# Kernel optimization log

Hardware: AMD Instinct MI355X
Metric: run time of the kernel (lower is better)

Reference implementation:

```python
import jax, jax.numpy as jnp
import numpy as np
from math import factorial

# irreps as (mul, l, parity): hidden = 64x0e + 32x1o + 16x2e (dim 240), edge = 1x0e + 1x1o (dim 4)
HIDDEN = [(64, 0, 1), (32, 1, -1), (16, 2, 1)]
EDGE = [(1, 0, 1), (1, 1, -1)]
N_LAYERS = 6
N_NODES = 10000
N_EDGES = 160000
N_GRAPHS = 64
IN_DIM = 3
LATENT = 128  # config.LATENT_DIM_GNN
W_STD = 0.1   # weight scale keeps 6 residual bilinear layers numerically stable

def _dim(ir):
    return sum(m * (2 * l + 1) for m, l, _ in ir)

def _slices(ir):
    out, o = [], 0
    for m, l, _ in ir:
        d = m * (2 * l + 1)
        out.append(slice(o, o + d))
        o += d
    return out

def _cg(j1, m1, j2, m2, j3, m3):
    # Condon-Shortley Clebsch-Gordan <j1 m1 j2 m2 | j3 m3> (Racah formula)
    if m1 + m2 != m3:
        return 0.0
    f = lambda n: float(factorial(n))
    pre = ((2 * j3 + 1) * f(j3 + j1 - j2) * f(j3 - j1 + j2) * f(j1 + j2 - j3) / f(j1 + j2 + j3 + 1)) ** 0.5
    pre *= (f(j3 + m3) * f(j3 - m3) * f(j1 - m1) * f(j1 + m1) * f(j2 - m2) * f(j2 + m2)) ** 0.5
    s = 0.0
    for k in range(j1 + j2 - j3 + 1):
        a = [k, j1 + j2 - j3 - k, j1 - m1 - k, j2 + m2 - k, j3 - j2 + m1 + k, j3 - j1 - m2 + k]
        if any(t < 0 for t in a):
            continue
        s += (-1) ** k / np.prod([f(t) for t in a])
    return pre * s

def _w3j_complex(l1, l2, l3):
    W = np.zeros((2 * l1 + 1, 2 * l2 + 1, 2 * l3 + 1))
    for m1 in range(-l1, l1 + 1):
        for m2 in range(-l2, l2 + 1):
            m3 = -(m1 + m2)
            if abs(m3) > l3:
                continue
            W[m1 + l1, m2 + l2, m3 + l3] = (-1) ** (l1 - l2 - m3) / np.sqrt(2 * l3 + 1) * _cg(l1, m1, l2, m2, l3, -m3)
    return W

def _A_real(l):
    # real SH in terms of complex SH: Y^r_m = sum_mu A[m, mu] Y_mu
    A = np.zeros((2 * l + 1, 2 * l + 1), dtype=complex)
    A[l, l] = 1.0
    for m in range(1, l + 1):
        A[l + m, l + m] = (-1) ** m / np.sqrt(2)
        A[l + m, l - m] = 1 / np.sqrt(2)
        A[l - m, l + m] = -1j * (-1) ** m / np.sqrt(2)
        A[l - m, l - m] = 1j / np.sqrt(2)
    return A

_W3J_CACHE = {}
def real_w3j(l1, l2, l3):
    key = (l1, l2, l3)
    if key not in _W3J_CACHE:
        T = np.einsum('ad,be,cf,def->abc', _A_real(l1), _A_real(l2), _A_real(l3), _w3j_complex(l1, l2, l3).astype(complex))
        T = np.real(T)  # exactly real when l1+l2+l3 is even (true for all paths here)
        _W3J_CACHE[key] = (T / np.linalg.norm(T)).astype(np.float32)
    return _W3J_CACHE[key]

def _paths(ir1, ir2, irout):
    ps = []
    for i1, (_, l1, p1) in enumerate(ir1):
        for i2, (_, l2, p2) in enumerate(ir2):
            for i3, (_, l3, p3) in enumerate(irout):
                if p3 == p1 * p2 and abs(l1 - l2) <= l3 <= l1 + l2:
                    ps.append((i1, i2, i3))
    return ps

MSG_PATHS = _paths(HIDDEN, EDGE, HIDDEN)
UPD_PATHS = _paths(HIDDEN, HIDDEN, HIDDEN)

def _tp_wsize(ir1, ir2, irout, paths):
    return sum(ir1[a][0] * ir2[b][0] * irout[c][0] for a, b, c in paths)

MSG_WSIZE = _tp_wsize(HIDDEN, EDGE, HIDDEN, MSG_PATHS)
UPD_WSIZE = _tp_wsize(HIDDEN, HIDDEN, HIDDEN, UPD_PATHS)
LIN_WSIZE = sum(m * m for m, _, _ in HIDDEN)

def tensor_product(x1, x2, w_flat, ir1, ir2, irout, paths):
    # FullyConnectedTensorProduct: per-path CG-coupled bilinear op with path normalization
    s1, s2, s3 = _slices(ir1), _slices(ir2), _slices(irout)
    npo = [0] * len(irout)
    for _, _, i3 in paths:
        npo[i3] += 1
    out = jnp.zeros((x1.shape[0], _dim(irout)), dtype=x1.dtype)
    off = 0
    for i1, i2, i3 in paths:
        m1, l1, _ = ir1[i1]; m2, l2, _ = ir2[i2]; m3, l3, _ = irout[i3]
        W = w_flat[off:off + m1 * m2 * m3].reshape(m1, m2, m3)
        off += m1 * m2 * m3
        C = jnp.asarray(real_w3j(l1, l2, l3), dtype=x1.dtype)
        a = x1[:, s1[i1]].reshape(-1, m1, 2 * l1 + 1)
        b = x2[:, s2[i2]].reshape(-1, m2, 2 * l2 + 1)
        alpha = 1.0 / np.sqrt(m1 * m2 * npo[i3])
        y = alpha * jnp.einsum('nui,nvj,uvw,ijk->nwk', a, b, W, C)
        out = out.at[:, s3[i3]].add(y.reshape(-1, m3 * (2 * l3 + 1)))
    return out

def irreps_linear(x, w_flat, ir):
    # e3nn Linear with identical in/out irreps: per-irrep mixing of multiplicities
    sl = _slices(ir)
    parts, off = [], 0
    for i, (m, l, _) in enumerate(ir):
        W = w_flat[off:off + m * m].reshape(m, m)
        off += m * m
        xi = x[:, sl[i]].reshape(-1, m, 2 * l + 1)
        parts.append((jnp.einsum('nui,uv->nvi', xi, W) / np.sqrt(m)).reshape(-1, m * (2 * l + 1)))
    return jnp.concatenate(parts, axis=-1)

def _forward(x, pos, w_init, w_tp_msg, w_lin_msg, w_tp_upd, w_lin_upd, w_final, edge_index, batch):
    row, col = edge_index[0], edge_index[1]
    r_vec = pos[row] - pos[col]                           # (E, 3)
    dist = jnp.linalg.norm(r_vec, axis=-1, keepdims=True)
    nvec = r_vec / jnp.maximum(dist, 1e-8)
    edge_attr = jnp.concatenate([dist, nvec], axis=-1)    # layer consumes [dist, r_vec] = 1x0e + 1x1o
    h = jnp.zeros((x.shape[0], _dim(HIDDEN)), dtype=x.dtype)
    h = h.at[:, :64].set(x @ w_init / np.sqrt(IN_DIM))    # initial Linear hits only 0e channels
    for L in range(N_LAYERS):
        hj = h[col]  # gather neighbor (source) features
        msg = tensor_product(hj, edge_attr, w_tp_msg[L], HIDDEN, EDGE, HIDDEN, MSG_PATHS) \
            + irreps_linear(hj, w_lin_msg[L], HIDDEN)
        agg = jax.ops.segment_sum(msg, row, num_segments=N_NODES)  # scatter-add aggregate
        upd = tensor_product(h, agg, w_tp_upd[L], HIDDEN, HIDDEN, HIDDEN, UPD_PATHS) \
            + irreps_linear(h, w_lin_upd[L], HIDDEN)
        h = h + upd  # residual
    scal = h[:, :64]  # 0e (invariant) channels
    cnt = jax.ops.segment_sum(jnp.ones((x.shape[0],), x.dtype), batch, num_segments=N_GRAPHS)
    pooled = jax.ops.segment_sum(scal, batch, num_segments=N_GRAPHS) / jnp.maximum(cnt, 1.0)[:, None]
    return pooled @ w_final / np.sqrt(64)

def setup_inputs() -> dict:
    key = jax.random.key(0)
    ks = jax.random.split(key, 10)
    return {
        'x': jax.random.normal(ks[0], (N_NODES, IN_DIM), jnp.float32),
        'pos': jax.random.normal(ks[1], (N_NODES, 3), jnp.float32),
        'w_init': jax.random.normal(ks[2], (IN_DIM, 64), jnp.float32),
        'w_tp_msg': jax.random.normal(ks[3], (N_LAYERS, MSG_WSIZE), jnp.float32) * W_STD,
        'w_lin_msg': jax.random.normal(ks[4], (N_LAYERS, LIN_WSIZE), jnp.float32) * W_STD,
        'w_tp_upd': jax.random.normal(ks[5], (N_LAYERS, UPD_WSIZE), jnp.float32) * W_STD,
        'w_lin_upd': jax.random.normal(ks[6], (N_LAYERS, LIN_WSIZE), jnp.float32) * W_STD,
        'w_final': jax.random.normal(ks[7], (64, LATENT), jnp.float32),
        'edge_index': jax.random.randint(ks[8], (2, N_EDGES), 0, N_NODES),
        'batch': jnp.sort(jax.random.randint(ks[9], (N_NODES,), 0, N_GRAPHS)),
    }

def reference(x, pos, w_init, w_tp_msg, w_lin_msg, w_tp_upd, w_lin_upd, w_final, edge_index, batch):
    return _forward(x, pos, w_init, w_tp_msg, w_lin_msg, w_tp_upd, w_lin_upd, w_final, edge_index, batch)
```

## Files before the change

### kernel.cpp

```cpp
#include <hip/hip_runtime.h>
#include <cmath>
#include <cstring>
#include <complex>

#define NN 10000
#define NE 160000
#define HD 240
#define ZD 912
#define NG 64
#define MSG_WS 10496
#define UPD_WS 561152
#define LIN_WS 5376

struct CMsgPre { float a000, a011, a110, a112, a211; float c101[9]; float c202[25]; };
struct CEdge   { float c011[9]; float c110[9]; float c112[45]; float c211[45]; };
struct CUpdS   { float s000; float c011[9]; float c022[25]; float c101[9]; float c202[25]; };
struct CUpdD   { float c110[9]; float c220[25]; };
struct CUpdP   { float c112[45]; float c121[45]; float c211[45]; float c222[125]; };


__global__ __launch_bounds__(256) void k_edge_attr(
    const float* __restrict__ pos, const int* __restrict__ ei, CEdge C,
    float* __restrict__ EA, float* __restrict__ CN) {
  int e = blockIdx.x * 256 + threadIdx.x;
  if (e >= NE) return;
  int r = ei[e], c = ei[NE + e];
  float dx = pos[r*3+0] - pos[c*3+0];
  float dy = pos[r*3+1] - pos[c*3+1];
  float dz = pos[r*3+2] - pos[c*3+2];
  float d = sqrtf(dx*dx + dy*dy + dz*dz);
  float inv = 1.0f / fmaxf(d, 1e-8f);
  float n0 = dx*inv, n1 = dy*inv, n2 = dz*inv;
  EA[e*4+0] = d; EA[e*4+1] = n0; EA[e*4+2] = n1; EA[e*4+3] = n2;
  float* cn = CN + (size_t)e*36;
#pragma unroll
  for (int k = 0; k < 3; k++)
    cn[k] = n0*C.c011[0*3+k] + n1*C.c011[1*3+k] + n2*C.c011[2*3+k];
#pragma unroll
  for (int i = 0; i < 3; i++)
    cn[3+i] = n0*C.c110[i*3+0] + n1*C.c110[i*3+1] + n2*C.c110[i*3+2];
#pragma unroll
  for (int i = 0; i < 3; i++)
#pragma unroll
    for (int k = 0; k < 5; k++)
      cn[6+i*5+k] = n0*C.c112[(i*3+0)*5+k] + n1*C.c112[(i*3+1)*5+k] + n2*C.c112[(i*3+2)*5+k];
#pragma unroll
  for (int i = 0; i < 5; i++)
#pragma unroll
    for (int k = 0; k < 3; k++)
      cn[21+i*3+k] = n0*C.c211[(i*3+0)*3+k] + n1*C.c211[(i*3+1)*3+k] + n2*C.c211[(i*3+2)*3+k];
}

__global__ __launch_bounds__(256) void k_h_init(
    const float* __restrict__ x, const float* __restrict__ wi, float* __restrict__ HT) {
  int n = blockIdx.x * 256 + threadIdx.x;
  int e = blockIdx.y;
  if (n >= NN) return;
  float v = 0.f;
  if (e < 64)
    v = (x[n*3+0]*wi[0*64+e] + x[n*3+1]*wi[64+e] + x[n*3+2]*wi[128+e]) * 0.57735026918962576f;
  HT[e*NN + n] = v;
}

__global__ __launch_bounds__(256) void k_node_pre(
    const float* __restrict__ HT, const float* __restrict__ Wm, const float* __restrict__ Wl,
    CMsgPre C, float* __restrict__ Z) {
  int n = blockIdx.x * 256 + threadIdx.x;
  int widx = blockIdx.y;
  if (n >= NN) return;
  float acc = 0.f;
  if (widx < 64) {
    int w = widx;
    for (int u = 0; u < 64; u++) acc += HT[u*NN+n] * Wm[u*64+w];
    acc *= C.a000;
  } else if (widx < 96) {
    int w = widx - 64;
    for (int u = 0; u < 64; u++) acc += HT[u*NN+n] * Wm[4096 + u*32+w];
    acc *= C.a011;
  } else if (widx < 192) {
    int t = widx - 96, w = t/3, k = t - w*3;
    for (int u = 0; u < 32; u++) {
      float g = HT[(64+u*3+0)*NN+n]*C.c101[0*3+k]
              + HT[(64+u*3+1)*NN+n]*C.c101[1*3+k]
              + HT[(64+u*3+2)*NN+n]*C.c101[2*3+k];
      acc += Wm[6144 + u*32+w] * g;
    }
  } else if (widx < 384) {
    int t = widx - 192, w = t/3, i = t - w*3;
    for (int u = 0; u < 32; u++) acc += HT[(64+u*3+i)*NN+n] * Wm[7168 + u*64+w];
    acc *= C.a110;
  } else if (widx < 432) {
    int t = widx - 384, w = t/3, i = t - w*3;
    for (int u = 0; u < 32; u++) acc += HT[(64+u*3+i)*NN+n] * Wm[9216 + u*16+w];
    acc *= C.a112;
  } else if (widx < 512) {
    int t = widx - 432, w = t/5, k = t - w*5;
    for (int u = 0; u < 16; u++) {
      float g = 0.f;
#pragma unroll
      for (int i = 0; i < 5; i++) g += HT[(160+u*5+i)*NN+n] * C.c202[i*5+k];
      acc += Wm[9728 + u*16+w] * g;
    }
  } else if (widx < 672) {
    int t = widx - 512, w = t/5, i = t - w*5;
    for (int u = 0; u < 16; u++) acc += HT[(160+u*5+i)*NN+n] * Wm[9984 + u*32+w];
    acc *= C.a211;
  } else {
    int e2 = widx - 672;
    if (e2 < 64) {
      for (int u = 0; u < 64; u++) acc += HT[u*NN+n] * Wl[u*64+e2];
      acc *= 0.125f;
    } else if (e2 < 160) {
      int t = e2 - 64, v = t/3, i = t - v*3;
      for (int u = 0; u < 32; u++) acc += HT[(64+u*3+i)*NN+n] * Wl[4096 + u*32+v];
      acc *= 0.17677669529663687f;
    } else {
      int t = e2 - 160, v = t/5, i = t - v*5;
      for (int u = 0; u < 16; u++) acc += HT[(160+u*5+i)*NN+n] * Wl[5120 + u*16+v];
      acc *= 0.25f;
    }
  }
  Z[(size_t)n*ZD + widx] = acc;
}

__global__ __launch_bounds__(256) void k_edge(
    const int* __restrict__ ei, const float* __restrict__ EA, const float* __restrict__ CN,
    const float* __restrict__ Z, float* __restrict__ AGG) {
  __shared__ float zsh[4][ZD];
  int lane = threadIdx.x & 63, wid = threadIdx.x >> 6;
  int wg = blockIdx.x * 4 + wid;
  int stride = gridDim.x * 4;
  int iters = (NE + stride - 1) / stride;
  for (int it = 0; it < iters; ++it) {
    int e = wg + it * stride;
    bool act = e < NE;
    int r = 0;
    float s = 0.f;
    const float* cn = CN;
    if (act) {
      r = ei[e];
      int c = ei[NE + e];
      s = EA[e*4];
      cn = CN + (size_t)e*36;
      const float* zr = Z + (size_t)c*ZD;
      for (int t = lane; t < ZD; t += 64) zsh[wid][t] = zr[t];
    }
    __syncthreads();
    if (act) {
      const float* z = zsh[wid];
#pragma unroll
      for (int j = 0; j < 4; j++) {
        int idx = lane + 64*j;
        if (idx < HD) {
          float y = z[672 + idx];
          if (idx < 64) {
            int w = idx;
            y += s * z[w];
#pragma unroll
            for (int i = 0; i < 3; i++) y += z[192 + w*3 + i] * cn[3+i];
          } else if (idx < 160) {
            int t = idx - 64, w = t/3, k = t - w*3;
            y += cn[k] * z[64 + w] + s * z[96 + t];
#pragma unroll
            for (int i = 0; i < 5; i++) y += z[512 + w*5 + i] * cn[21 + i*3 + k];
          } else {
            int t = idx - 160, w = t/5, k = t - w*5;
            y += s * z[432 + t];
#pragma unroll
            for (int i = 0; i < 3; i++) y += z[384 + w*3 + i] * cn[6 + i*5 + k];
          }
          atomicAdd(&AGG[(size_t)r*HD + idx], y);
        }
      }
    }
    __syncthreads();
  }
}

__global__ __launch_bounds__(256) void k_transpose(
    const float* __restrict__ A_nm, float* __restrict__ A_t) {
  int n = blockIdx.x * 256 + threadIdx.x;
  int e = blockIdx.y;
  if (n >= NN) return;
  A_t[e*NN + n] = A_nm[(size_t)n*HD + e];
}

__global__ __launch_bounds__(128, 2) void k_upd(
    const float* __restrict__ A,
    const float* __restrict__ B,
    const float* __restrict__ W,
    CUpdS CS, CUpdD CD, CUpdP CP,
    float* __restrict__ UPD) {
  __shared__ float4 lds4[1024];
  const int tid = threadIdx.x;
  const int n0 = blockIdx.x * 256 + tid;
  const int n1 = n0 + 128;
  const bool ok0 = n0 < NN, ok1 = n1 < NN;
  const int nc0 = ok0 ? n0 : NN - 1;
  const int nc1 = ok1 ? n1 : NN - 1;
  const int py = blockIdx.y;

#define LDA2(dst, e) { int _e=(e); dst.x = A[_e*NN+nc0]; dst.y = A[_e*NN+nc1]; }
#define LDB2(dst, e) { int _e=(e); dst.x = B[_e*NN+nc0]; dst.y = B[_e*NN+nc1]; }

  if (py < 16) {
    const int w04 = py;
    float2 y[4];
#pragma unroll
    for (int w = 0; w < 4; w++) y[w] = make_float2(0.f, 0.f);

    {
      const float4* W4 = (const float4*)W;
      for (int uc = 0; uc < 4; ++uc) {
        __syncthreads();
        for (int t = tid; t < 1024; t += 128) lds4[t] = W4[(uc*1024 + t)*16 + w04];
        __syncthreads();
        float2 ha[16];
#pragma unroll
        for (int u = 0; u < 16; ++u) {
          LDA2(ha[u], uc*16 + u);
          ha[u].x *= CS.s000; ha[u].y *= CS.s000;
        }
        for (int v = 0; v < 64; ++v) {
          float2 bv; LDB2(bv, v);
#pragma unroll
          for (int u = 0; u < 16; ++u) {
            float4 wl = lds4[u*64 + v];
            float px = ha[u].x * bv.x, qx = ha[u].y * bv.y;
            y[0].x += px*wl.x; y[0].y += qx*wl.x;
            y[1].x += px*wl.y; y[1].y += qx*wl.y;
            y[2].x += px*wl.z; y[2].y += qx*wl.z;
            y[3].x += px*wl.w; y[3].y += qx*wl.w;
          }
        }
      }
    }

    {
      const float4* W4 = (const float4*)(W + 409600);
      __syncthreads();
      for (int t = tid; t < 1024; t += 128) lds4[t] = W4[t*16 + w04];
      __syncthreads();
      for (int uc = 0; uc < 4; ++uc) {
        float2 a[8][3];
#pragma unroll
        for (int u = 0; u < 8; ++u)
#pragma unroll
          for (int i = 0; i < 3; ++i) LDA2(a[u][i], 64 + (uc*8+u)*3 + i);
        for (int v = 0; v < 32; ++v) {
          float2 b[3];
#pragma unroll
          for (int j = 0; j < 3; ++j) LDB2(b[j], 64 + v*3 + j);
          float2 bt[3];
#pragma unroll
          for (int i = 0; i < 3; ++i) {
            bt[i].x = CD.c110[i*3+0]*b[0].x + CD.c110[i*3+1]*b[1].x + CD.c110[i*3+2]*b[2].x;
            bt[i].y = CD.c110[i*3+0]*b[0].y + CD.c110[i*3+1]*b[1].y + CD.c110[i*3+2]*b[2].y;
          }
#pragma unroll
          for (int u = 0; u < 8; ++u) {
            float Dx = a[u][0].x*bt[0].x + a[u][1].x*bt[1].x + a[u][2].x*bt[2].x;
            float Dy = a[u][0].y*bt[0].y + a[u][1].y*bt[1].y + a[u][2].y*bt[2].y;
            float4 wl = lds4[(uc*8+u)*32 + v];
            y[0].x += Dx*wl.x; y[0].y += Dy*wl.x;
            y[1].x += Dx*wl.y; y[1].y += Dy*wl.y;
            y[2].x += Dx*wl.z; y[2].y += Dy*wl.z;
            y[3].x += Dx*wl.w; y[3].y += Dy*wl.w;
          }
        }
      }
    }

    {
      const float4* W4 = (const float4*)(W + 540672);
      __syncthreads();
      for (int t = tid; t < 256; t += 128) lds4[t] = W4[t*16 + w04];
      __syncthreads();
      for (int uc = 0; uc < 4; ++uc) {
        float2 a[4][5];
#pragma unroll
        for (int u = 0; u < 4; ++u)
#pragma unroll
          for (int i = 0; i < 5; ++i) LDA2(a[u][i], 160 + (uc*4+u)*5 + i);
        for (int v = 0; v < 16; ++v) {
          float2 b[5];
#pragma unroll
          for (int j = 0; j < 5; ++j) LDB2(b[j], 160 + v*5 + j);
          float2 bt[5];
#pragma unroll
          for (int i = 0; i < 5; ++i) {
            float tx = 0.f, ty = 0.f;
#pragma unroll
            for (int j = 0; j < 5; ++j) { tx += CD.c220[i*5+j]*b[j].x; ty += CD.c220[i*5+j]*b[j].y; }
            bt[i].x = tx; bt[i].y = ty;
          }
#pragma unroll
          for (int u = 0; u < 4; ++u) {
            float Dx = 0.f, Dy = 0.f;
#pragma unroll
            for (int i = 0; i < 5; ++i) { Dx += a[u][i].x*bt[i].x; Dy += a[u][i].y*bt[i].y; }
            float4 wl = lds4[(uc*4+u)*16 + v];
            y[0].x += Dx*wl.x; y[0].y += Dy*wl.x;
            y[1].x += Dx*wl.y; y[1].y += Dy*wl.y;
            y[2].x += Dx*wl.z; y[2].y += Dy*wl.z;
            y[3].x += Dx*wl.w; y[3].y += Dy*wl.w;
          }
        }
      }
    }

#pragma unroll
    for (int w = 0; w < 4; ++w) {
      if (ok0) UPD[(py*4 + w)*NN + n0] = y[w].x;
      if (ok1) UPD[(py*4 + w)*NN + n1] = y[w].y;
    }

  } else if (py < 24) {
    const int w04 = py - 16;
    float2 y[4][3];
#pragma unroll
    for (int w = 0; w < 4; w++)
#pragma unroll
      for (int k = 0; k < 3; k++) y[w][k] = make_float2(0.f, 0.f);

    {
      const float4* W4 = (const float4*)(W + 262144);
      for (int uc = 0; uc < 2; ++uc) {
        __syncthreads();
        for (int t = tid; t < 1024; t += 128) lds4[t] = W4[(uc*1024 + t)*8 + w04];
        __syncthreads();
        float2 a[32];
#pragma unroll
        for (int u = 0; u < 32; ++u) LDA2(a[u], uc*32 + u);
        for (int v = 0; v < 32; ++v) {
          float2 b[3];
#pragma unroll
          for (int j = 0; j < 3; ++j) LDB2(b[j], 64 + v*3 + j);
          float2 bc[3];
#pragma unroll
          for (int k = 0; k < 3; ++k) {
            bc[k].x = b[0].x*CS.c011[k] + b[1].x*CS.c011[3+k] + b[2].x*CS.c011[6+k];
            bc[k].y = b[0].y*CS.c011[k] + b[1].y*CS.c011[3+k] + b[2].y*CS.c011[6+k];
          }
          float2 g[4];
#pragma unroll
          for (int w = 0; w < 4; w++) g[w] = make_float2(0.f, 0.f);
#pragma unroll
          for (int u = 0; u < 32; ++u) {
            float4 wl = lds4[u*32 + v];
            g[0].x += a[u].x*wl.x; g[0].y += a[u].y*wl.x;
            g[1].x += a[u].x*wl.y; g[1].y += a[u].y*wl.y;
            g[2].x += a[u].x*wl.z; g[2].y += a[u].y*wl.z;
            g[3].x += a[u].x*wl.w; g[3].y += a[u].y*wl.w;
          }
#pragma unroll
          for (int w = 0; w < 4; ++w)
#pragma unroll
            for (int k = 0; k < 3; ++k) {
              y[w][k].x += bc[k].x*g[w].x; y[w][k].y += bc[k].y*g[w].y;
            }
        }
      }
    }

    {
      const float4* W4 = (const float4*)(W + 344064);
      for (int uc = 0; uc < 2; ++uc) {
        __syncthreads();
        for (int t = tid; t < 1024; t += 128) lds4[t] = W4[(uc*1024 + t)*8 + w04];
        __syncthreads();
        for (int vc = 0; vc < 4; ++vc) {
          float2 bv[16];
#pragma unroll
          for (int v2 = 0; v2 < 16; ++v2) LDB2(bv[v2], vc*16 + v2);
          for (int u = 0; u < 16; ++u) {
            float2 aa[3];
#pragma unroll
            for (int i = 0; i < 3; ++i) LDA2(aa[i], 64 + (uc*16+u)*3 + i);
            float2 ac[3];
#pragma unroll
            for (int k = 0; k < 3; ++k) {
              ac[k].x = aa[0].x*CS.c101[k] + aa[1].x*CS.c101[3+k] + aa[2].x*CS.c101[6+k];
              ac[k].y = aa[0].y*CS.c101[k] + aa[1].y*CS.c101[3+k] + aa[2].y*CS.c101[6+k];
            }
            float2 gp[4];
#pragma unroll
            for (int w = 0; w < 4; w++) gp[w] = make_float2(0.f, 0.f);
#pragma unroll
            for (int v2 = 0; v2 < 16; ++v2) {
              float4 wl = lds4[u*64 + vc*16 + v2];
              gp[0].x += bv[v2].x*wl.x; gp[0].y += bv[v2].y*wl.x;
              gp[1].x += bv[v2].x*wl.y; gp[1].y += bv[v2].y*wl.y;
              gp[2].x += bv[v2].x*wl.z; gp[2].y += bv[v2].y*wl.z;
              gp[3].x += bv[v2].x*wl.w; gp[3].y += bv[v2].y*wl.w;
            }
#pragma unroll
            for (int w = 0; w < 4; ++w)
#pragma unroll
              for (int k = 0; k < 3; ++k) {
                y[w][k].x += ac[k].x*gp[w].x; y[w][k].y += ac[k].y*gp[w].y;
              }
          }
        }
      }
    }

    {
      const float4* W4 = (const float4*)(W + 491520);
      __syncthreads();
      for (int t = tid; t < 512; t += 128) lds4[t] = W4[t*8 + w04];
      __syncthreads();
      for (int uc = 0; uc < 4; ++uc) {
        float2 a[8][3];
#pragma unroll
        for (int u = 0; u < 8; ++u)
#pragma unroll
          for (int i = 0; i < 3; ++i) LDA2(a[u][i], 64 + (uc*8+u)*3 + i);
        for (int v = 0; v < 16; ++v) {
          float2 b[5];
#pragma unroll
          for (int j = 0; j < 5; ++j) LDB2(b[j], 160 + v*5 + j);
          float2 bt[3][3];
#pragma unroll
          for (int i = 0; i < 3; ++i)
#pragma unroll
            for (int k = 0; k < 3; ++k) {
              float tx = 0.f, ty = 0.f;
#pragma unroll
              for (int j = 0; j < 5; ++j) { tx += b[j].x*CP.c121[(i*5+j)*3+k]; ty += b[j].y*CP.c121[(i*5+j)*3+k]; }
              bt[i][k].x = tx; bt[i][k].y = ty;
            }
#pragma unroll
          for (int u = 0; u < 8; ++u) {
            float2 P[3];
#pragma unroll
            for (int k = 0; k < 3; ++k) {
              P[k].x = a[u][0].x*bt[0][k].x + a[u][1].x*bt[1][k].x + a[u][2].x*bt[2][k].x;
              P[k].y = a[u][0].y*bt[0][k].y + a[u][1].y*bt[1][k].y + a[u][2].y*bt[2][k].y;
            }
            float4 wl = lds4[(uc*8+u)*16 + v];
#pragma unroll
            for (int k = 0; k < 3; ++k) {
              y[0][k].x += P[k].x*wl.x; y[0][k].y += P[k].y*wl.x;
              y[1][k].x += P[k].x*wl.y; y[1][k].y += P[k].y*wl.y;
              y[2][k].x += P[k].x*wl.z; y[2][k].y += P[k].y*wl.z;
              y[3][k].x += P[k].x*wl.w; y[3][k].y += P[k].y*wl.w;
            }
          }
        }
      }
    }

    {
      const float4* W4 = (const float4*)(W + 524288);
      __syncthreads();
      for (int t = tid; t < 512; t += 128) lds4[t] = W4[t*8 + w04];
      __syncthreads();
      for (int uc = 0; uc < 2; ++uc) {
        float2 a[8][5];
#pragma unroll
        for (int u = 0; u < 8; ++u)
#pragma unroll
          for (int i = 0; i < 5; ++i) LDA2(a[u][i], 160 + (uc*8+u)*5 + i);
        for (int v = 0; v < 32; ++v) {
          float2 b[3];
#pragma unroll
          for (int j = 0; j < 3; ++j) LDB2(b[j], 64 + v*3 + j);
          float2 bt[5][3];
#pragma unroll
          for (int i = 0; i < 5; ++i)
#pragma unroll
            for (int k = 0; k < 3; ++k) {
              bt[i][k].x = b[0].x*CP.c211[(i*3+0)*3+k] + b[1].x*CP.c211[(i*3+1)*3+k] + b[2].x*CP.c211[(i*3+2)*3+k];
              bt[i][k].y = b[0].y*CP.c211[(i*3+0)*3+k] + b[1].y*CP.c211[(i*3+1)*3+k] + b[2].y*CP.c211[(i*3+2)*3+k];
            }
#pragma unroll
          for (int u = 0; u < 8; ++u) {
            float2 P[3];
#pragma unroll
            for (int k = 0; k < 3; ++k) {
              float tx = 0.f, ty = 0.f;
#pragma unroll
              for (int i = 0; i < 5; ++i) { tx += a[u][i].x*bt[i][k].x; ty += a[u][i].y*bt[i][k].y; }
              P[k].x = tx; P[k].y = ty;
            }
            float4 wl = lds4[(uc*8+u)*32 + v];
#pragma unroll
            for (int k = 0; k < 3; ++k) {
              y[0][k].x += P[k].x*wl.x; y[0][k].y += P[k].y*wl.x;
              y[1][k].x += P[k].x*wl.y; y[1][k].y += P[k].y*wl.y;
              y[2][k].x += P[k].x*wl.z; y[2][k].y += P[k].y*wl.z;
              y[3][k].x += P[k].x*wl.w; y[3][k].y += P[k].y*wl.w;
            }
          }
        }
      }
    }

#pragma unroll
    for (int w = 0; w < 4; ++w)
#pragma unroll
      for (int k = 0; k < 3; ++k) {
        int e = 64 + (w04*4 + w)*3 + k;
        if (ok0) UPD[e*NN + n0] = y[w][k].x;
        if (ok1) UPD[e*NN + n1] = y[w][k].y;
      }

  } else {
    const int w04 = py - 24;
    float2 y[4][5];
#pragma unroll
    for (int w = 0; w < 4; w++)
#pragma unroll
      for (int k = 0; k < 5; k++) y[w][k] = make_float2(0.f, 0.f);

    {
      const float4* W4 = (const float4*)(W + 327680);
      __syncthreads();
      for (int t = tid; t < 1024; t += 128) lds4[t] = W4[t*4 + w04];
      __syncthreads();
      for (int uc = 0; uc < 4; ++uc) {
        float2 a[16];
#pragma unroll
        for (int u = 0; u < 16; ++u) LDA2(a[u], uc*16 + u);
        for (int v = 0; v < 16; ++v) {
          float2 b[5];
#pragma unroll
          for (int j = 0; j < 5; ++j) LDB2(b[j], 160 + v*5 + j);
          float2 bc[5];
#pragma unroll
          for (int k = 0; k < 5; ++k) {
            float tx = 0.f, ty = 0.f;
#pragma unroll
            for (int j = 0; j < 5; ++j) { tx += b[j].x*CS.c022[j*5+k]; ty += b[j].y*CS.c022[j*5+k]; }
            bc[k].x = tx; bc[k].y = ty;
          }
          float2 g[4];
#pragma unroll
          for (int w = 0; w < 4; w++) g[w] = make_float2(0.f, 0.f);
#pragma unroll
          for (int u = 0; u < 16; ++u) {
            float4 wl = lds4[(uc*16+u)*16 + v];
            g[0].x += a[u].x*wl.x; g[0].y += a[u].y*wl.x;
            g[1].x += a[u].x*wl.y; g[1].y += a[u].y*wl.y;
            g[2].x += a[u].x*wl.z; g[2].y += a[u].y*wl.z;
            g[3].x += a[u].x*wl.w; g[3].y += a[u].y*wl.w;
          }
#pragma unroll
          for (int w = 0; w < 4; ++w)
#pragma unroll
            for (int k = 0; k < 5; ++k) {
              y[w][k].x += bc[k].x*g[w].x; y[w][k].y += bc[k].y*g[w].y;
            }
        }
      }
    }

    {
      const float4* W4 = (const float4*)(W + 507904);
      __syncthreads();
      for (int t = tid; t < 1024; t += 128) lds4[t] = W4[t*4 + w04];
      __syncthreads();
      for (int vc = 0; vc < 4; ++vc) {
        float2 bv[16];
#pragma unroll
        for (int v2 = 0; v2 < 16; ++v2) LDB2(bv[v2], vc*16 + v2);
        for (int u = 0; u < 16; ++u) {
          float2 aa[5];
#pragma unroll
          for (int i = 0; i < 5; ++i) LDA2(aa[i], 160 + u*5 + i);
          float2 ac[5];
#pragma unroll
          for (int k = 0; k < 5; ++k) {
            float tx = 0.f, ty = 0.f;
#pragma unroll
            for (int i = 0; i < 5; ++i) { tx += aa[i].x*CS.c202[i*5+k]; ty += aa[i].y*CS.c202[i*5+k]; }
            ac[k].x = tx; ac[k].y = ty;
          }
          float2 gp[4];
#pragma unroll
          for (int w = 0; w < 4; w++) gp[w] = make_float2(0.f, 0.f);
#pragma unroll
          for (int v2 = 0; v2 < 16; ++v2) {
            float4 wl = lds4[u*64 + vc*16 + v2];
            gp[0].x += bv[v2].x*wl.x; gp[0].y += bv[v2].y*wl.x;
            gp[1].x += bv[v2].x*wl.y; gp[1].y += bv[v2].y*wl.y;
            gp[2].x += bv[v2].x*wl.z; gp[2].y += bv[v2].y*wl.z;
            gp[3].x += bv[v2].x*wl.w; gp[3].y += bv[v2].y*wl.w;
          }
#pragma unroll
          for (int w = 0; w < 4; ++w)
#pragma unroll
            for (int k = 0; k < 5; ++k) {
              y[w][k].x += ac[k].x*gp[w].x; y[w][k].y += ac[k].y*gp[w].y;
            }
        }
      }
    }

    {
      const float4* W4 = (const float4*)(W + 475136);
      __syncthreads();
      for (int t = tid; t < 1024; t += 128) lds4[t] = W4[t*4 + w04];
      __syncthreads();
      for (int uc = 0; uc < 4; ++uc) {
        float2 a[8][3];
#pragma unroll
        for (int u = 0; u < 8; ++u)
#pragma unroll
          for (int i = 0; i < 3; ++i) LDA2(a[u][i], 64 + (uc*8+u)*3 + i);
        for (int v = 0; v < 32; ++v) {
          float2 b[3];
#pragma unroll
          for (int j = 0; j < 3; ++j) LDB2(b[j], 64 + v*3 + j);
          float2 bt[3][5];
#pragma unroll
          for (int i = 0; i < 3; ++i)
#pragma unroll
            for (int k = 0; k < 5; ++k) {
              bt[i][k].x = b[0].x*CP.c112[(i*3+0)*5+k] + b[1].x*CP.c112[(i*3+1)*5+k] + b[2].x*CP.c112[(i*3+2)*5+k];
              bt[i][k].y = b[0].y*CP.c112[(i*3+0)*5+k] + b[1].y*CP.c112[(i*3+1)*5+k] + b[2].y*CP.c112[(i*3+2)*5+k];
            }
#pragma unroll
          for (int u = 0; u < 8; ++u) {
            float2 P[5];
#pragma unroll
            for (int k = 0; k < 5; ++k) {
              P[k].x = a[u][0].x*bt[0][k].x + a[u][1].x*bt[1][k].x + a[u][2].x*bt[2][k].x;
              P[k].y = a[u][0].y*bt[0][k].y + a[u][1].y*bt[1][k].y + a[u][2].y*bt[2][k].y;
            }
            float4 wl = lds4[(uc*8+u)*32 + v];
#pragma unroll
            for (int k = 0; k < 5; ++k) {
              y[0][k].x += P[k].x*wl.x; y[0][k].y += P[k].y*wl.x;
              y[1][k].x += P[k].x*wl.y; y[1][k].y += P[k].y*wl.y;
              y[2][k].x += P[k].x*wl.z; y[2][k].y += P[k].y*wl.z;
              y[3][k].x += P[k].x*wl.w; y[3][k].y += P[k].y*wl.w;
            }
          }
        }
      }
    }

    {
      const float4* W4 = (const float4*)(W + 557056);
      __syncthreads();
      for (int t = tid; t < 256; t += 128) lds4[t] = W4[t*4 + w04];
      __syncthreads();
      for (int v = 0; v < 16; ++v) {
        float2 b[5];
#pragma unroll
        for (int j = 0; j < 5; ++j) LDB2(b[j], 160 + v*5 + j);
        float2 bt[5][5];
#pragma unroll
        for (int i = 0; i < 5; ++i)
#pragma unroll
          for (int k = 0; k < 5; ++k) {
            float tx = 0.f, ty = 0.f;
#pragma unroll
            for (int j = 0; j < 5; ++j) { tx += b[j].x*CP.c222[(i*5+j)*5+k]; ty += b[j].y*CP.c222[(i*5+j)*5+k]; }
            bt[i][k].x = tx; bt[i][k].y = ty;
          }
        for (int u = 0; u < 16; ++u) {
          float2 aa[5];
#pragma unroll
          for (int i = 0; i < 5; ++i) LDA2(aa[i], 160 + u*5 + i);
          float2 P[5];
#pragma unroll
          for (int k = 0; k < 5; ++k) {
            float tx = 0.f, ty = 0.f;
#pragma unroll
            for (int i = 0; i < 5; ++i) { tx += aa[i].x*bt[i][k].x; ty += aa[i].y*bt[i][k].y; }
            P[k].x = tx; P[k].y = ty;
          }
          float4 wl = lds4[u*16 + v];
#pragma unroll
          for (int k = 0; k < 5; ++k) {
            y[0][k].x += P[k].x*wl.x; y[0][k].y += P[k].y*wl.x;
            y[1][k].x += P[k].x*wl.y; y[1][k].y += P[k].y*wl.y;
            y[2][k].x += P[k].x*wl.z; y[2][k].y += P[k].y*wl.z;
            y[3][k].x += P[k].x*wl.w; y[3][k].y += P[k].y*wl.w;
          }
        }
      }
    }

#pragma unroll
    for (int w = 0; w < 4; ++w)
#pragma unroll
      for (int k = 0; k < 5; ++k) {
        int e = 160 + (w04*4 + w)*5 + k;
        if (ok0) UPD[e*NN + n0] = y[w][k].x;
        if (ok1) UPD[e*NN + n1] = y[w][k].y;
      }
  }
#undef LDA2
#undef LDB2
}

__global__ __launch_bounds__(256) void k_apply(
    const float* __restrict__ Hsrc, const float* __restrict__ UPD,
    const float* __restrict__ Wl, float* __restrict__ Hdst) {
  int n = blockIdx.x * 256 + threadIdx.x;
  int e = blockIdx.y;
  if (n >= NN) return;
  float lin = 0.f;
  if (e < 64) {
    for (int u = 0; u < 64; u++) lin += Hsrc[u*NN+n] * Wl[u*64+e];
    lin *= 0.125f;
  } else if (e < 160) {
    int t = e - 64, v = t/3, i = t - v*3;
    for (int u = 0; u < 32; u++) lin += Hsrc[(64+u*3+i)*NN+n] * Wl[4096 + u*32+v];
    lin *= 0.17677669529663687f;
  } else {
    int t = e - 160, v = t/5, i = t - v*5;
    for (int u = 0; u < 16; u++) lin += Hsrc[(160+u*5+i)*NN+n] * Wl[5120 + u*16+v];
    lin *= 0.25f;
  }
  Hdst[e*NN + n] = Hsrc[e*NN + n] + UPD[e*NN + n] + lin;
}

__global__ __launch_bounds__(256) void k_cnt(const int* __restrict__ batch, float* __restrict__ CNT) {
  int n = blockIdx.x * 256 + threadIdx.x;
  if (n >= NN) return;
  atomicAdd(&CNT[batch[n]], 1.0f);
}

__global__ __launch_bounds__(256) void k_pool(
    const float* __restrict__ HT, const int* __restrict__ batch, float* __restrict__ POOL) {
  int n = blockIdx.x * 256 + threadIdx.x;
  int w = blockIdx.y;
  if (n >= NN) return;
  atomicAdd(&POOL[batch[n]*64 + w], HT[w*NN + n]);
}

__global__ __launch_bounds__(256) void k_out(
    const float* __restrict__ POOL, const float* __restrict__ CNT,
    const float* __restrict__ wf, float* __restrict__ out) {
  int tid = blockIdx.x * 256 + threadIdx.x;
  if (tid >= NG * 128) return;
  int g = tid >> 7, d = tid & 127;
  float inv = 1.0f / fmaxf(CNT[g], 1.0f);
  float acc = 0.f;
  for (int w = 0; w < 64; w++) acc += POOL[g*64 + w] * wf[w*128 + d];
  out[tid] = acc * inv * 0.125f;
}

typedef std::complex<double> cd;
static double hfact(int nn) { double f = 1; for (int i = 2; i <= nn; i++) f *= i; return f; }
static double hcg(int j1,int m1,int j2,int m2,int j3,int m3) {
  if (m1 + m2 != m3) return 0.0;
  double pre = sqrt((2*j3+1) * hfact(j3+j1-j2) * hfact(j3-j1+j2) * hfact(j1+j2-j3) / hfact(j1+j2+j3+1));
  pre *= sqrt(hfact(j3+m3)*hfact(j3-m3)*hfact(j1-m1)*hfact(j1+m1)*hfact(j2-m2)*hfact(j2+m2));
  double s = 0;
  for (int k = 0; k <= j1+j2-j3; k++) {
    int a1=j1+j2-j3-k, a2=j1-m1-k, a3=j2+m2-k, a4=j3-j2+m1+k, a5=j3-j1-m2+k;
    if (a1<0||a2<0||a3<0||a4<0||a5<0) continue;
    s += ((k&1)?-1.0:1.0) / (hfact(k)*hfact(a1)*hfact(a2)*hfact(a3)*hfact(a4)*hfact(a5));
  }
  return pre * s;
}
static void hA(int l, cd A[5][5]) {
  for (int r = 0; r < 5; r++) for (int c = 0; c < 5; c++) A[r][c] = cd(0,0);
  A[l][l] = cd(1,0);
  for (int m = 1; m <= l; m++) {
    double sg = (m & 1) ? -1.0 : 1.0;
    A[l+m][l+m] = cd(sg/sqrt(2.0), 0);
    A[l+m][l-m] = cd(1.0/sqrt(2.0), 0);
    A[l-m][l+m] = cd(0, -sg/sqrt(2.0));
    A[l-m][l-m] = cd(0, 1.0/sqrt(2.0));
  }
}
static void hw3j(int l1, int l2, int l3, double* out) {
  int n1 = 2*l1+1, n2 = 2*l2+1, n3 = 2*l3+1;
  double Wc[5][5][5]; memset(Wc, 0, sizeof Wc);
  for (int m1 = -l1; m1 <= l1; m1++) for (int m2 = -l2; m2 <= l2; m2++) {
    int m3 = -(m1+m2);
    if (m3 < -l3 || m3 > l3) continue;
    int ex = l1 - l2 - m3;
    double sg = (ex % 2 == 0) ? 1.0 : -1.0;
    Wc[m1+l1][m2+l2][m3+l3] = sg / sqrt((double)(2*l3+1)) * hcg(l1,m1,l2,m2,l3,-m3);
  }
  cd A1[5][5], A2[5][5], A3[5][5];
  hA(l1,A1); hA(l2,A2); hA(l3,A3);
  double nrm = 0;
  for (int a = 0; a < n1; a++) for (int b = 0; b < n2; b++) for (int c = 0; c < n3; c++) {
    cd acc(0,0);
    for (int d = 0; d < n1; d++) for (int e = 0; e < n2; e++) for (int f = 0; f < n3; f++) {
      double w = Wc[d][e][f];
      if (w == 0.0) continue;
      acc += A1[a][d] * A2[b][e] * A3[c][f] * w;
    }
    out[(a*n2+b)*n3+c] = acc.real();
    nrm += acc.real() * acc.real();
  }
  nrm = sqrt(nrm);
  for (int i = 0; i < n1*n2*n3; i++) out[i] /= nrm;
}

extern "C" void kernel_launch(void* const* d_in, const int* in_sizes, int n_in,
                              void* d_out, int out_size, void* d_ws, size_t ws_size,
                              hipStream_t stream) {
  const float* x        = (const float*)d_in[0];
  const float* pos      = (const float*)d_in[1];
  const float* w_init   = (const float*)d_in[2];
  const float* w_tp_msg = (const float*)d_in[3];
  const float* w_lin_msg= (const float*)d_in[4];
  const float* w_tp_upd = (const float*)d_in[5];
  const float* w_lin_upd= (const float*)d_in[6];
  const float* w_final  = (const float*)d_in[7];
  const int*   ei       = (const int*)d_in[8];
  const int*   batch    = (const int*)d_in[9];
  float* out = (float*)d_out;
  float* ws  = (float*)d_ws;

  float* EA     = ws;
  float* CN     = EA + 640000;
  float* HTA    = CN + 5760000;
  float* HTB    = HTA + 2400000;
  float* Z      = HTB + 2400000;
  float* AGG_NM = Z + 9120000;
  float* UPD_T  = AGG_NM + 2400000;
  float* AGG_T  = UPD_T + 2400000;
  float* POOL   = AGG_T + 2400000;
  float* CNT    = POOL + 4096;

  double C000d[1], C011d[9], C101d[9], C110d[9], C112d[45], C022d[25],
         C202d[25], C121d[45], C211d[45], C220d[25], C222d[125];
  hw3j(0,0,0,C000d); hw3j(0,1,1,C011d); hw3j(1,0,1,C101d); hw3j(1,1,0,C110d);
  hw3j(1,1,2,C112d); hw3j(0,2,2,C022d); hw3j(2,0,2,C202d); hw3j(1,2,1,C121d);
  hw3j(2,1,1,C211d); hw3j(2,2,0,C220d); hw3j(2,2,2,C222d);

  CMsgPre cmsg;
  cmsg.a000 = (float)(C000d[0] / sqrt(128.0));
  cmsg.a011 = (float)(1.0 / sqrt(192.0));
  cmsg.a110 = (float)(1.0 / sqrt(64.0));
  cmsg.a112 = (float)(1.0 / sqrt(64.0));
  cmsg.a211 = (float)(1.0 / sqrt(48.0));
  for (int i = 0; i < 9;  i++) cmsg.c101[i] = (float)(C101d[i] / sqrt(96.0));
  for (int i = 0; i < 25; i++) cmsg.c202[i] = (float)(C202d[i] / sqrt(32.0));

  CEdge ce;
  for (int i = 0; i < 9;  i++) ce.c011[i] = (float)C011d[i];
  for (int i = 0; i < 9;  i++) ce.c110[i] = (float)C110d[i];
  for (int i = 0; i < 45; i++) ce.c112[i] = (float)C112d[i];
  for (int i = 0; i < 45; i++) ce.c211[i] = (float)C211d[i];

  CUpdS cus;
  cus.s000 = (float)(C000d[0] / sqrt(64.0*64.0*3.0));
  for (int i = 0; i < 9;  i++) cus.c011[i] = (float)(C011d[i] / sqrt(64.0*32.0*4.0));
  for (int i = 0; i < 25; i++) cus.c022[i] = (float)(C022d[i] / sqrt(64.0*16.0*4.0));
  for (int i = 0; i < 9;  i++) cus.c101[i] = (float)(C101d[i] / sqrt(32.0*64.0*4.0));
  for (int i = 0; i < 25; i++) cus.c202[i] = (float)(C202d[i] / sqrt(16.0*64.0*4.0));

  CUpdD cud;
  for (int i = 0; i < 9;  i++) cud.c110[i] = (float)(C110d[i] / sqrt(32.0*32.0*3.0));
  for (int i = 0; i < 25; i++) cud.c220[i] = (float)(C220d[i] / sqrt(16.0*16.0*3.0));

  CUpdP cup;
  for (int i = 0; i < 45;  i++) cup.c112[i] = (float)(C112d[i] / sqrt(32.0*32.0*4.0));
  for (int i = 0; i < 45;  i++) cup.c121[i] = (float)(C121d[i] / sqrt(32.0*16.0*4.0));
  for (int i = 0; i < 45;  i++) cup.c211[i] = (float)(C211d[i] / sqrt(16.0*32.0*4.0));
  for (int i = 0; i < 125; i++) cup.c222[i] = (float)(C222d[i] / sqrt(16.0*16.0*4.0));

  k_edge_attr<<<(NE+255)/256, 256, 0, stream>>>(pos, ei, ce, EA, CN);
  k_h_init<<<dim3(40, HD), 256, 0, stream>>>(x, w_init, HTA);

  float* cur = HTA;
  float* nxt = HTB;
  for (int L = 0; L < 6; L++) {
    hipMemsetAsync(AGG_NM, 0, (size_t)2400000 * sizeof(float), stream);
    k_node_pre<<<dim3(40, ZD), 256, 0, stream>>>(cur, w_tp_msg + (size_t)L*MSG_WS,
                                                 w_lin_msg + (size_t)L*LIN_WS, cmsg, Z);
    k_edge<<<1280, 256, 0, stream>>>(ei, EA, CN, Z, AGG_NM);
    k_transpose<<<dim3(40, HD), 256, 0, stream>>>(AGG_NM, AGG_T);
    const float* Wu = w_tp_upd + (size_t)L*UPD_WS;
    k_upd<<<dim3(40, 28), 128, 0, stream>>>(cur, AGG_T, Wu, cus, cud, cup, UPD_T);
    k_apply<<<dim3(40, HD), 256, 0, stream>>>(cur, UPD_T, w_lin_upd + (size_t)L*LIN_WS, nxt);
    float* tmp = cur; cur = nxt; nxt = tmp;
  }

  hipMemsetAsync(POOL, 0, (size_t)(4096 + 64) * sizeof(float), stream);
  k_cnt<<<(NN+255)/256, 256, 0, stream>>>(batch, CNT);
  k_pool<<<dim3(40, 64), 256, 0, stream>>>(cur, batch, POOL);
  k_out<<<32, 256, 0, stream>>>(POOL, CNT, w_final, out);
}
```

Before: 5.464 ms.

## Split k_upd output channels two per block to double grid parallelism

The update tensor-product kernel now computes 2 output channels per block instead of 4 for the scalar and vector outputs, raising the grid from 28 to 52 y-blocks. Weights are staged as float2 rather than float4 in shared memory, and the launch bound asks for 4 blocks per CU to cut register pressure. The aim is more blocks and waves to fill the GPU, since the old grid of 40x28 blocks underused it. The cost is that each block reloads the same A/B node features and redoes the Clebsch-Gordan contractions, so global reads grow for the same output.

Result: slower. 8.935 ms (+63.5%).

```diff
diff --git a/kernel.cpp b/kernel.cpp
--- a/kernel.cpp
+++ b/kernel.cpp
@@ -185,13 +185,14 @@
   A_t[e*NN + n] = A_nm[(size_t)n*HD + e];
 }
 
-__global__ __launch_bounds__(128, 2) void k_upd(
+__global__ __launch_bounds__(128, 4) void k_upd(
     const float* __restrict__ A,
     const float* __restrict__ B,
     const float* __restrict__ W,
     CUpdS CS, CUpdD CD, CUpdP CP,
     float* __restrict__ UPD) {
   __shared__ float4 lds4[1024];
+  float2* lds2 = (float2*)lds4;
   const int tid = threadIdx.x;
   const int n0 = blockIdx.x * 256 + tid;
   const int n1 = n0 + 128;
@@ -199,481 +200,407 @@
   const int nc0 = ok0 ? n0 : NN - 1;
   const int nc1 = ok1 ? n1 : NN - 1;
   const int py = blockIdx.y;
+  const float2* W2 = (const float2*)W;
 
 #define LDA2(dst, e) { int _e=(e); dst.x = A[_e*NN+nc0]; dst.y = A[_e*NN+nc1]; }
 #define LDB2(dst, e) { int _e=(e); dst.x = B[_e*NN+nc0]; dst.y = B[_e*NN+nc1]; }
 
-  if (py < 16) {
-    const int w04 = py;
-    float2 y[4];
-#pragma unroll
-    for (int w = 0; w < 4; w++) y[w] = make_float2(0.f, 0.f);
-
-    {
-      const float4* W4 = (const float4*)W;
-      for (int uc = 0; uc < 4; ++uc) {
-        __syncthreads();
-        for (int t = tid; t < 1024; t += 128) lds4[t] = W4[(uc*1024 + t)*16 + w04];
-        __syncthreads();
-        float2 ha[16];
+  if (py < 32) {
+    const int w02 = py;
+    float2 y[2];
+    y[0] = make_float2(0.f, 0.f); y[1] = make_float2(0.f, 0.f);
+
+    for (int uc = 0; uc < 4; ++uc) {
+      __syncthreads();
+      for (int t = tid; t < 1024; t += 128)
+        lds2[t] = W2[((uc*16 + (t >> 6)) * 64 + (t & 63)) * 32 + w02];
+      __syncthreads();
+      float2 ha[16];
+#pragma unroll
+      for (int u = 0; u < 16; ++u) {
+        LDA2(ha[u], uc*16 + u);
+        ha[u].x *= CS.s000; ha[u].y *= CS.s000;
+      }
+#pragma unroll 2
+      for (int v = 0; v < 64; ++v) {
+        float2 bv; LDB2(bv, v);
 #pragma unroll
         for (int u = 0; u < 16; ++u) {
-          LDA2(ha[u], uc*16 + u);
-          ha[u].x *= CS.s000; ha[u].y *= CS.s000;
-        }
-        for (int v = 0; v < 64; ++v) {
-          float2 bv; LDB2(bv, v);
-#pragma unroll
-          for (int u = 0; u < 16; ++u) {
-            float4 wl = lds4[u*64 + v];
-            float px = ha[u].x * bv.x, qx = ha[u].y * bv.y;
-            y[0].x += px*wl.x; y[0].y += qx*wl.x;
-            y[1].x += px*wl.y; y[1].y += qx*wl.y;
-            y[2].x += px*wl.z; y[2].y += qx*wl.z;
-            y[3].x += px*wl.w; y[3].y += qx*wl.w;
-          }
-        }
-      }
-    }
-
-    {
-      const float4* W4 = (const float4*)(W + 409600);
-      __syncthreads();
-      for (int t = tid; t < 1024; t += 128) lds4[t] = W4[t*16 + w04];
-      __syncthreads();
-      for (int uc = 0; uc < 4; ++uc) {
-        float2 a[8][3];
-#pragma unroll
-        for (int u = 0; u < 8; ++u)
-#pragma unroll
-          for (int i = 0; i < 3; ++i) LDA2(a[u][i], 64 + (uc*8+u)*3 + i);
-        for (int v = 0; v < 32; ++v) {
-          float2 b[3];
-#pragma unroll
-          for (int j = 0; j < 3; ++j) LDB2(b[j], 64 + v*3 + j);
-          float2 bt[3];
-#pragma unroll
-          for (int i = 0; i < 3; ++i) {
-            bt[i].x = CD.c110[i*3+0]*b[0].x + CD.c110[i*3+1]*b[1].x + CD.c110[i*3+2]*b[2].x;
-            bt[i].y = CD.c110[i*3+0]*b[0].y + CD.c110[i*3+1]*b[1].y + CD.c110[i*3+2]*b[2].y;
-          }
-#pragma unroll
-          for (int u = 0; u < 8; ++u) {
-            float Dx = a[u][0].x*bt[0].x + a[u][1].x*bt[1].x + a[u][2].x*bt[2].x;
-            float Dy = a[u][0].y*bt[0].y + a[u][1].y*bt[1].y + a[u][2].y*bt[2].y;
-            float4 wl = lds4[(uc*8+u)*32 + v];
-            y[0].x += Dx*wl.x; y[0].y += Dy*wl.x;
-            y[1].x += Dx*wl.y; y[1].y += Dy*wl.y;
-            y[2].x += Dx*wl.z; y[2].y += Dy*wl.z;
-            y[3].x += Dx*wl.w; y[3].y += Dy*wl.w;
-          }
-        }
-      }
-    }
-
-    {
-      const float4* W4 = (const float4*)(W + 540672);
-      __syncthreads();
-      for (int t = tid; t < 256; t += 128) lds4[t] = W4[t*16 + w04];
-      __syncthreads();
-      for (int uc = 0; uc < 4; ++uc) {
-        float2 a[4][5];
-#pragma unroll
-        for (int u = 0; u < 4; ++u)
-#pragma unroll
-          for (int i = 0; i < 5; ++i) LDA2(a[u][i], 160 + (uc*4+u)*5 + i);
-        for (int v = 0; v < 16; ++v) {
-          float2 b[5];
-#pragma unroll
-          for (int j = 0; j < 5; ++j) LDB2(b[j], 160 + v*5 + j);
-          float2 bt[5];
-#pragma unroll
-          for (int i = 0; i < 5; ++i) {
+          float2 wl = lds2[u*64 + v];
+          float px = ha[u].x * bv.x, qx = ha[u].y * bv.y;
+          y[0].x += px*wl.x; y[0].y += qx*wl.x;
+          y[1].x += px*wl.y; y[1].y += qx*wl.y;
+        }
+      }
+    }
+
+    __syncthreads();
+    for (int t = tid; t < 1024; t += 128)
+      lds2[t] = W2[204800 + t*32 + w02];
+    __syncthreads();
+    for (int uc = 0; uc < 4; ++uc) {
+      float2 a[8][3];
+#pragma unroll
+      for (int u = 0; u < 8; ++u)
+#pragma unroll
+        for (int i = 0; i < 3; ++i) LDA2(a[u][i], 64 + (uc*8+u)*3 + i);
+#pragma unroll 2
+      for (int v = 0; v < 32; ++v) {
+        float2 b[3];
+#pragma unroll
+        for (int j = 0; j < 3; ++j) LDB2(b[j], 64 + v*3 + j);
+        float2 bt[3];
+#pragma unroll
+        for (int i = 0; i < 3; ++i) {
+          bt[i].x = CD.c110[i*3+0]*b[0].x + CD.c110[i*3+1]*b[1].x + CD.c110[i*3+2]*b[2].x;
+          bt[i].y = CD.c110[i*3+0]*b[0].y + CD.c110[i*3+1]*b[1].y + CD.c110[i*3+2]*b[2].y;
+        }
+#pragma unroll
+        for (int u = 0; u < 8; ++u) {
+          float Dx = a[u][0].x*bt[0].x + a[u][1].x*bt[1].x + a[u][2].x*bt[2].x;
+          float Dy = a[u][0].y*bt[0].y + a[u][1].y*bt[1].y + a[u][2].y*bt[2].y;
+          float2 wl = lds2[(uc*8+u)*32 + v];
+          y[0].x += Dx*wl.x; y[0].y += Dy*wl.x;
+          y[1].x += Dx*wl.y; y[1].y += Dy*wl.y;
+        }
+      }
+    }
+
+    __syncthreads();
+    for (int t = tid; t < 256; t += 128)
+      lds2[t] = W2[270336 + t*32 + w02];
+    __syncthreads();
+    for (int uc = 0; uc < 4; ++uc) {
+      float2 a[4][5];
+#pragma unroll
+      for (int u = 0; u < 4; ++u)
+#pragma unroll
+        for (int i = 0; i < 5; ++i) LDA2(a[u][i], 160 + (uc*4+u)*5 + i);
+      for (int v = 0; v < 16; ++v) {
+        float2 b[5];
+#pragma unroll
+        for (int j = 0; j < 5; ++j) LDB2(b[j], 160 + v*5 + j);
+        float2 bt[5];
+#pragma unroll
+        for (int i = 0; i < 5; ++i) {
+          float tx = 0.f, ty = 0.f;
+#pragma unroll
+          for (int j = 0; j < 5; ++j) { tx += CD.c220[i*5+j]*b[j].x; ty += CD.c220[i*5+j]*b[j].y; }
+          bt[i].x = tx; bt[i].y = ty;
+        }
+#pragma unroll
+        for (int u = 0; u < 4; ++u) {
+          float Dx = 0.f, Dy = 0.f;
+#pragma unroll
+          for (int i = 0; i < 5; ++i) { Dx += a[u][i].x*bt[i].x; Dy += a[u][i].y*bt[i].y; }
+          float2 wl = lds2[(uc*4+u)*16 + v];
+          y[0].x += Dx*wl.x; y[0].y += Dy*wl.x;
+          y[1].x += Dx*wl.y; y[1].y += Dy*wl.y;
+        }
+      }
+    }
+
+#pragma unroll
+    for (int w = 0; w < 2; ++w) {
+      if (ok0) UPD[(py*2 + w)*NN + n0] = y[w].x;
+      if (ok1) UPD[(py*2 + w)*NN + n1] = y[w].y;
+    }
+
+  } else if (py < 48) {
+    const int w02 = py - 32;
+    float2 y[2][3];
+#pragma unroll
+    for (int w = 0; w < 2; w++)
+#pragma unroll
+      for (int k = 0; k < 3; k++) y[w][k] = make_float2(0.f, 0.f);
+
+    __syncthreads();
+    for (int t = tid; t < 2048; t += 128)
+      lds2[t] = W2[131072 + t*16 + w02];
+    __syncthreads();
+    for (int uc = 0; uc < 4; ++uc) {
+      float2 a[16];
+#pragma unroll
+      for (int u = 0; u < 16; ++u) LDA2(a[u], uc*16 + u);
+#pragma unroll 2
+      for (int v = 0; v < 32; ++v) {
+        float2 b[3];
+#pragma unroll
+        for (int j = 0; j < 3; ++j) LDB2(b[j], 64 + v*3 + j);
+        float2 bc[3];
+#pragma unroll
+        for (int k = 0; k < 3; ++k) {
+          bc[k].x = b[0].x*CS.c011[k] + b[1].x*CS.c011[3+k] + b[2].x*CS.c011[6+k];
+          bc[k].y = b[0].y*CS.c011[k] + b[1].y*CS.c011[3+k] + b[2].y*CS.c011[6+k];
+        }
+        float2 g[2];
+        g[0] = make_float2(0.f, 0.f); g[1] = make_float2(0.f, 0.f);
+#pragma unroll
+        for (int u = 0; u < 16; ++u) {
+          float2 wl = lds2[(uc*16+u)*32 + v];
+          g[0].x += a[u].x*wl.x; g[0].y += a[u].y*wl.x;
+          g[1].x += a[u].x*wl.y; g[1].y += a[u].y*wl.y;
+        }
+#pragma unroll
+        for (int w = 0; w < 2; ++w)
+#pragma unroll
+          for (int k = 0; k < 3; ++k) {
+            y[w][k].x += bc[k].x*g[w].x; y[w][k].y += bc[k].y*g[w].y;
+          }
+      }
+    }
+
+    __syncthreads();
+    for (int t = tid; t < 2048; t += 128)
+      lds2[t] = W2[172032 + t*16 + w02];
+    __syncthreads();
+    for (int uc = 0; uc < 2; ++uc) {
+      for (int vc = 0; vc < 4; ++vc) {
+        float2 bv[16];
+#pragma unroll
+        for (int v2 = 0; v2 < 16; ++v2) LDB2(bv[v2], vc*16 + v2);
+        for (int u = 0; u < 16; ++u) {
+          float2 aa[3];
+#pragma unroll
+          for (int i = 0; i < 3; ++i) LDA2(aa[i], 64 + (uc*16+u)*3 + i);
+          float2 ac[3];
+#pragma unroll
+          for (int k = 0; k < 3; ++k) {
+            ac[k].x = aa[0].x*CS.c101[k] + aa[1].x*CS.c101[3+k] + aa[2].x*CS.c101[6+k];
+            ac[k].y = aa[0].y*CS.c101[k] + aa[1].y*CS.c101[3+k] + aa[2].y*CS.c101[6+k];
+          }
+          float2 gp[2];
+          gp[0] = make_float2(0.f, 0.f); gp[1] = make_float2(0.f, 0.f);
+#pragma unroll
+          for (int v2 = 0; v2 < 16; ++v2) {
+            float2 wl = lds2[(uc*16+u)*64 + vc*16 + v2];
+            gp[0].x += bv[v2].x*wl.x; gp[0].y += bv[v2].y*wl.x;
+            gp[1].x += bv[v2].x*wl.y; gp[1].y += bv[v2].y*wl.y;
+          }
+#pragma unroll
+          for (int w = 0; w < 2; ++w)
+#pragma unroll
+            for (int k = 0; k < 3; ++k) {
+              y[w][k].x += ac[k].x*gp[w].x; y[w][k].y += ac[k].y*gp[w].y;
+            }
+        }
+      }
+    }
+
+    __syncthreads();
+    for (int t = tid; t < 512; t += 128)
+      lds2[t] = W2[245760 + t*16 + w02];
+    __syncthreads();
+    for (int uc = 0; uc < 4; ++uc) {
+      float2 a[8][3];
+#pragma unroll
+      for (int u = 0; u < 8; ++u)
+#pragma unroll
+        for (int i = 0; i < 3; ++i) LDA2(a[u][i], 64 + (uc*8+u)*3 + i);
+      for (int v = 0; v < 16; ++v) {
+        float2 b[5];
+#pragma unroll
+        for (int j = 0; j < 5; ++j) LDB2(b[j], 160 + v*5 + j);
+        float2 bt[3][3];
+#pragma unroll
+        for (int i = 0; i < 3; ++i)
+#pragma unroll
+          for (int k = 0; k < 3; ++k) {
             float tx = 0.f, ty = 0.f;
 #pragma unroll
-            for (int j = 0; j < 5; ++j) { tx += CD.c220[i*5+j]*b[j].x; ty += CD.c220[i*5+j]*b[j].y; }
-            bt[i].x = tx; bt[i].y = ty;
-          }
-#pragma unroll
-          for (int u = 0; u < 4; ++u) {
-            float Dx = 0.f, Dy = 0.f;
-#pragma unroll
-            for (int i = 0; i < 5; ++i) { Dx += a[u][i].x*bt[i].x; Dy += a[u][i].y*bt[i].y; }
-            float4 wl = lds4[(uc*4+u)*16 + v];
-            y[0].x += Dx*wl.x; y[0].y += Dy*wl.x;
-            y[1].x += Dx*wl.y; y[1].y += Dy*wl.y;
-            y[2].x += Dx*wl.z; y[2].y += Dy*wl.z;
-            y[3].x += Dx*wl.w; y[3].y += Dy*wl.w;
-          }
-        }
-      }
-    }
-
-#pragma unroll
-    for (int w = 0; w < 4; ++w) {
-      if (ok0) UPD[(py*4 + w)*NN + n0] = y[w].x;
-      if (ok1) UPD[(py*4 + w)*NN + n1] = y[w].y;
-    }
-
-  } else if (py < 24) {
-    const int w04 = py - 16;
-    float2 y[4][3];
-#pragma unroll
-    for (int w = 0; w < 4; w++)
-#pragma unroll
-      for (int k = 0; k < 3; k++) y[w][k] = make_float2(0.f, 0.f);
-
-    {
-      const float4* W4 = (const float4*)(W + 262144);
-      for (int uc = 0; uc < 2; ++uc) {
-        __syncthreads();
-        for (int t = tid; t < 1024; t += 128) lds4[t] = W4[(uc*1024 + t)*8 + w04];
-        __syncthreads();
-        float2 a[32];
-#pragma unroll
-        for (int u = 0; u < 32; ++u) LDA2(a[u], uc*32 + u);
-        for (int v = 0; v < 32; ++v) {
-          float2 b[3];
-#pragma unroll
-          for (int j = 0; j < 3; ++j) LDB2(b[j], 64 + v*3 + j);
-          float2 bc[3];
+            for (int j = 0; j < 5; ++j) { tx += b[j].x*CP.c121[(i*5+j)*3+k]; ty += b[j].y*CP.c121[(i*5+j)*3+k]; }
+            bt[i][k].x = tx; bt[i][k].y = ty;
+          }
+#pragma unroll
+        for (int u = 0; u < 8; ++u) {
+          float2 P[3];
 #pragma unroll
           for (int k = 0; k < 3; ++k) {
-            bc[k].x = b[0].x*CS.c011[k] + b[1].x*CS.c011[3+k] + b[2].x*CS.c011[6+k];
-            bc[k].y = b[0].y*CS.c011[k] + b[1].y*CS.c011[3+k] + b[2].y*CS.c011[6+k];
-          }
-          float2 g[4];
-#pragma unroll
-          for (int w = 0; w < 4; w++) g[w] = make_float2(0.f, 0.f);
-#pragma unroll
-          for (int u = 0; u < 32; ++u) {
-            float4 wl = lds4[u*32 + v];
-            g[0].x += a[u].x*wl.x; g[0].y += a[u].y*wl.x;
-            g[1].x += a[u].x*wl.y; g[1].y += a[u].y*wl.y;
-            g[2].x += a[u].x*wl.z; g[2].y += a[u].y*wl.z;
-            g[3].x += a[u].x*wl.w; g[3].y += a[u].y*wl.w;
-          }
-#pragma unroll
-          for (int w = 0; w < 4; ++w)
-#pragma unroll
-            for (int k = 0; k < 3; ++k) {
-              y[w][k].x += bc[k].x*g[w].x; y[w][k].y += bc[k].y*g[w].y;
-            }
-        }
-      }
-    }
-
-    {
-      const float4* W4 = (const float4*)(W + 344064);
-      for (int uc = 0; uc < 2; ++uc) {
-        __syncthreads();
-        for (int t = tid; t < 1024; t += 128) lds4[t] = W4[(uc*1024 + t)*8 + w04];
-        __syncthreads();
-        for (int vc = 0; vc < 4; ++vc) {
-          float2 bv[16];
-#pragma unroll
-          for (int v2 = 0; v2 < 16; ++v2) LDB2(bv[v2], vc*16 + v2);
-          for (int u = 0; u < 16; ++u) {
-            float2 aa[3];
-#pragma unroll
-            for (int i = 0; i < 3; ++i) LDA2(aa[i], 64 + (uc*16+u)*3 + i);
-            float2 ac[3];
-#pragma unroll
-            for (int k = 0; k < 3; ++k) {
-              ac[k].x = aa[0].x*CS.c101[k] + aa[1].x*CS.c101[3+k] + aa[2].x*CS.c101[6+k];
-              ac[k].y = aa[0].y*CS.c101[k] + aa[1].y*CS.c101[3+k] + aa[2].y*CS.c101[6+k];
-            }
-            float2 gp[4];
-#pragma unroll
-            for (int w = 0; w < 4; w++) gp[w] = make_float2(0.f, 0.f);
-#pragma unroll
-            for (int v2 = 0; v2 < 16; ++v2) {
-              float4 wl = lds4[u*64 + vc*16 + v2];
-              gp[0].x += bv[v2].x*wl.x; gp[0].y += bv[v2].y*wl.x;
-              gp[1].x += bv[v2].x*wl.y; gp[1].y += bv[v2].y*wl.y;
-              gp[2].x += bv[v2].x*wl.z; gp[2].y += bv[v2].y*wl.z;
-              gp[3].x += bv[v2].x*wl.w; gp[3].y += bv[v2].y*wl.w;
-            }
-#pragma unroll
-            for (int w = 0; w < 4; ++w)
-#pragma unroll
-              for (int k = 0; k < 3; ++k) {
-                y[w][k].x += ac[k].x*gp[w].x; y[w][k].y += ac[k].y*gp[w].y;
-              }
-          }
-        }
-      }
-    }
-
-    {
-      const float4* W4 = (const float4*)(W + 491520);
-      __syncthreads();
-      for (int t = tid; t < 512; t += 128) lds4[t] = W4[t*8 + w04];
-      __syncthreads();
-      for (int uc = 0; uc < 4; ++uc) {
-        float2 a[8][3];
-#pragma unroll
-        for (int u = 0; u < 8; ++u)
-#pragma unroll
-          for (int i = 0; i < 3; ++i) LDA2(a[u][i], 64 + (uc*8+u)*3 + i);
-        for (int v = 0; v < 16; ++v) {
-          float2 b[5];
-#pragma unroll
-          for (int j = 0; j < 5; ++j) LDB2(b[j], 160 + v*5 + j);
-          float2 bt[3][3];
-#pragma unroll
-          for (int i = 0; i < 3; ++i)
-#pragma unroll
-            for (int k = 0; k < 3; ++k) {
-              float tx = 0.f, ty = 0.f;
-#pragma unroll
-              for (int j = 0; j < 5; ++j) { tx += b[j].x*CP.c121[(i*5+j)*3+k]; ty += b[j].y*CP.c121[(i*5+j)*3+k]; }
-              bt[i][k].x = tx; bt[i][k].y = ty;
-            }
-#pragma unroll
-          for (int u = 0; u < 8; ++u) {
-            float2 P[3];
-#pragma unroll
-            for (int k = 0; k < 3; ++k) {
-              P[k].x = a[u][0].x*bt[0][k].x + a[u][1].x*bt[1][k].x + a[u][2].x*bt[2][k].x;
-              P[k].y = a[u][0].y*bt[0][k].y + a[u][1].y*bt[1][k].y + a[u][2].y*bt[2][k].y;
-            }
-            float4 wl = lds4[(uc*8+u)*16 + v];
-#pragma unroll
-            for (int k = 0; k < 3; ++k) {
-              y[0][k].x += P[k].x*wl.x; y[0][k].y += P[k].y*wl.x;
-              y[1][k].x += P[k].x*wl.y; y[1][k].y += P[k].y*wl.y;
-              y[2][k].x += P[k].x*wl.z; y[2][k].y += P[k].y*wl.z;
-              y[3][k].x += P[k].x*wl.w; y[3][k].y += P[k].y*wl.w;
-            }
-          }
-        }
-      }
-    }
-
-    {
-      const float4* W4 = (const float4*)(W + 524288);
-      __syncthreads();
-      for (int t = tid; t < 512; t += 128) lds4[t] = W4[t*8 + w04];
-      __syncthreads();
-      for (int uc = 0; uc < 2; ++uc) {
-        float2 a[8][5];
-#pragma unroll
-        for (int u = 0; u < 8; ++u)
-#pragma unroll
-          for (int i = 0; i < 5; ++i) LDA2(a[u][i], 160 + (uc*8+u)*5 + i);
-        for (int v = 0; v < 32; ++v) {
-          float2 b[3];
-#pragma unroll
-          for (int j = 0; j < 3; ++j) LDB2(b[j], 64 + v*3 + j);
-          float2 bt[5][3];
-#pragma unroll
-          for (int i = 0; i < 5; ++i)
-#pragma unroll
-            for (int k = 0; k < 3; ++k) {
-              bt[i][k].x = b[0].x*CP.c211[(i*3+0)*3+k] + b[1].x*CP.c211[(i*3+1)*3+k] + b[2].x*CP.c211[(i*3+2)*3+k];
-              bt[i][k].y = b[0].y*CP.c211[(i*3+0)*3+k] + b[1].y*CP.c211[(i*3+1)*3+k] + b[2].y*CP.c211[(i*3+2)*3+k];
-            }
-#pragma unroll
-          for (int u = 0; u < 8; ++u) {
-            float2 P[3];
-#pragma unroll
-            for (int k = 0; k < 3; ++k) {
-              float tx = 0.f, ty = 0.f;
-#pragma unroll
-              for (int i = 0; i < 5; ++i) { tx += a[u][i].x*bt[i][k].x; ty += a[u][i].y*bt[i][k].y; }
-              P[k].x = tx; P[k].y = ty;
-            }
-            float4 wl = lds4[(uc*8+u)*32 + v];
-#pragma unroll
-            for (int k = 0; k < 3; ++k) {
-              y[0][k].x += P[k].x*wl.x; y[0][k].y += P[k].y*wl.x;
-              y[1][k].x += P[k].x*wl.y; y[1][k].y += P[k].y*wl.y;
-              y[2][k].x += P[k].x*wl.z; y[2][k].y += P[k].y*wl.z;
-              y[3][k].x += P[k].x*wl.w; y[3][k].y += P[k].y*wl.w;
-            }
-          }
-        }
-      }
-    }
-
-#pragma unroll
-    for (int w = 0; w < 4; ++w)
+            P[k].x = a[u][0].x*bt[0][k].x + a[u][1].x*bt[1][k].x + a[u][2].x*bt[2][k].x;
+            P[k].y = a[u][0].y*bt[0][k].y + a[u][1].y*bt[1][k].y + a[u][2].y*bt[2][k].y;
+          }
+          float2 wl = lds2[(uc*8+u)*16 + v];
+#pragma unroll
+          for (int k = 0; k < 3; ++k) {
+            y[0][k].x += P[k].x*wl.x; y[0][k].y += P[k].y*wl.x;
+            y[1][k].x += P[k].x*wl.y; y[1][k].y += P[k].y*wl.y;
+          }
+        }
+      }
+    }
+
+    __syncthreads();
+    for (int t = tid; t < 512; t += 128)
+      lds2[t] = W2[262144 + t*16 + w02];
+    __syncthreads();
+    for (int uc = 0; uc < 2; ++uc) {
+      float2 a[8][5];
+#pragma unroll
+      for (int u = 0; u < 8; ++u)
+#pragma unroll
+        for (int i = 0; i < 5; ++i) LDA2(a[u][i], 160 + (uc*8+u)*5 + i);
+#pragma unroll 2
+      for (int v = 0; v < 32; ++v) {
+        float2 b[3];
+#pragma unroll
+        for (int j = 0; j < 3; ++j) LDB2(b[j], 64 + v*3 + j);
+        float2 bt[5][3];
+#pragma unroll
+        for (int i = 0; i < 5; ++i)
+#pragma unroll
+          for (int k = 0; k < 3; ++k) {
+            bt[i][k].x = b[0].x*CP.c211[(i*3+0)*3+k] + b[1].x*CP.c211[(i*3+1)*3+k] + b[2].x*CP.c211[(i*3+2)*3+k];
+            bt[i][k].y = b[0].y*CP.c211[(i*3+0)*3+k] + b[1].y*CP.c211[(i*3+1)*3+k] + b[2].y*CP.c211[(i*3+2)*3+k];
+          }
+#pragma unroll
+        for (int u = 0; u < 8; ++u) {
+          float2 P[3];
+#pragma unroll
+          for (int k = 0; k < 3; ++k) {
+            float tx = 0.f, ty = 0.f;
+#pragma unroll
+            for (int i = 0; i < 5; ++i) { tx += a[u][i].x*bt[i][k].x; ty += a[u][i].y*bt[i][k].y; }
+            P[k].x = tx; P[k].y = ty;
+          }
+          float2 wl = lds2[(uc*8+u)*32 + v];
+#pragma unroll
+          for (int k = 0; k < 3; ++k) {
+            y[0][k].x += P[k].x*wl.x; y[0][k].y += P[k].y*wl.x;
+            y[1][k].x += P[k].x*wl.y; y[1][k].y += P[k].y*wl.y;
+          }
+        }
+      }
+    }
+
+#pragma unroll
+    for (int w = 0; w < 2; ++w)
 #pragma unroll
       for (int k = 0; k < 3; ++k) {
-        int e = 64 + (w04*4 + w)*3 + k;
+        int e = 64 + (w02*2 + w)*3 + k;
         if (ok0) UPD[e*NN + n0] = y[w][k].x;
         if (ok1) UPD[e*NN + n1] = y[w][k].y;
       }
 
   } else {
-    const int w04 = py - 24;
+    const int w04 = py - 48;
     float2 y[4][5];
 #pragma unroll
     for (int w = 0; w < 4; w++)
 #pragma unroll
       for (int k = 0; k < 5; k++) y[w][k] = make_float2(0.f, 0.f);
 
-    {
-      const float4* W4 = (const float4*)(W + 327680);
-      __syncthreads();
-      for (int t = tid; t < 1024; t += 128) lds4[t] = W4[t*4 + w04];
-      __syncthreads();
-      for (int uc = 0; uc < 4; ++uc) {
-        float2 a[16];
-#pragma unroll
-        for (int u = 0; u < 16; ++u) LDA2(a[u], uc*16 + u);
-        for (int v = 0; v < 16; ++v) {
-          float2 b[5];
-#pragma unroll
-          for (int j = 0; j < 5; ++j) LDB2(b[j], 160 + v*5 + j);
-          float2 bc[5];
-#pragma unroll
-          for (int k = 0; k < 5; ++k) {
-            float tx = 0.f, ty = 0.f;
-#pragma unroll
-            for (int j = 0; j < 5; ++j) { tx += b[j].x*CS.c022[j*5+k]; ty += b[j].y*CS.c022[j*5+k]; }
-            bc[k].x = tx; bc[k].y = ty;
-          }
-          float2 g[4];
-#pragma unroll
-          for (int w = 0; w < 4; w++) g[w] = make_float2(0.f, 0.f);
-#pragma unroll
-          for (int u = 0; u < 16; ++u) {
-            float4 wl = lds4[(uc*16+u)*16 + v];
-            g[0].x += a[u].x*wl.x; g[0].y += a[u].y*wl.x;
-            g[1].x += a[u].x*wl.y; g[1].y += a[u].y*wl.y;
-            g[2].x += a[u].x*wl.z; g[2].y += a[u].y*wl.z;
-            g[3].x += a[u].x*wl.w; g[3].y += a[u].y*wl.w;
-          }
-#pragma unroll
-          for (int w = 0; w < 4; ++w)
-#pragma unroll
-            for (int k = 0; k < 5; ++k) {
-              y[w][k].x += bc[k].x*g[w].x; y[w][k].y += bc[k].y*g[w].y;
-            }
-        }
-      }
-    }
-
-    {
-      const float4* W4 = (const float4*)(W + 507904);
-      __syncthreads();
-      for (int t = tid; t < 1024; t += 128) lds4[t] = W4[t*4 + w04];
-      __syncthreads();
-      for (int vc = 0; vc < 4; ++vc) {
-        float2 bv[16];
-#pragma unroll
-        for (int v2 = 0; v2 < 16; ++v2) LDB2(bv[v2], vc*16 + v2);
-        for (int u = 0; u < 16; ++u) {
-          float2 aa[5];
-#pragma unroll
-          for (int i = 0; i < 5; ++i) LDA2(aa[i], 160 + u*5 + i);
-          float2 ac[5];
-#pragma unroll
-          for (int k = 0; k < 5; ++k) {
-            float tx = 0.f, ty = 0.f;
-#pragma unroll
-            for (int i = 0; i < 5; ++i) { tx += aa[i].x*CS.c202[i*5+k]; ty += aa[i].y*CS.c202[i*5+k]; }
-            ac[k].x = tx; ac[k].y = ty;
-          }
-          float2 gp[4];
-#pragma unroll
-          for (int w = 0; w < 4; w++) gp[w] = make_float2(0.f, 0.f);
-#pragma unroll
-          for (int v2 = 0; v2 < 16; ++v2) {
-            float4 wl = lds4[u*64 + vc*16 + v2];
-            gp[0].x += bv[v2].x*wl.x; gp[0].y += bv[v2].y*wl.x;
-            gp[1].x += bv[v2].x*wl.y; gp[1].y += bv[v2].y*wl.y;
-            gp[2].x += bv[v2].x*wl.z; gp[2].y += bv[v2].y*wl.z;
-            gp[3].x += bv[v2].x*wl.w; gp[3].y += bv[v2].y*wl.w;
-          }
-#pragma unroll
-          for (int w = 0; w < 4; ++w)
-#pragma unroll
-            for (int k = 0; k < 5; ++k) {
-              y[w][k].x += ac[k].x*gp[w].x; y[w][k].y += ac[k].y*gp[w].y;
-            }
-        }
-      }
-    }
-
-    {
-      const float4* W4 = (const float4*)(W + 475136);
-      __syncthreads();
-      for (int t = tid; t < 1024; t += 128) lds4[t] = W4[t*4 + w04];
-      __syncthreads();
-      for (int uc = 0; uc < 4; ++uc) {
-        float2 a[8][3];
-#pragma unroll
-        for (int u = 0; u < 8; ++u)
-#pragma unroll
-          for (int i = 0; i < 3; ++i) LDA2(a[u][i], 64 + (uc*8+u)*3 + i);
-        for (int v = 0; v < 32; ++v) {
-          float2 b[3];
-#pragma unroll
-          for (int j = 0; j < 3; ++j) LDB2(b[j], 64 + v*3 + j);
-          float2 bt[3][5];
-#pragma unroll
-          for (int i = 0; i < 3; ++i)
-#pragma unroll
-            for (int k = 0; k < 5; ++k) {
-              bt[i][k].x = b[0].x*CP.c112[(i*3+0)*5+k] + b[1].x*CP.c112[(i*3+1)*5+k] + b[2].x*CP.c112[(i*3+2)*5+k];
-              bt[i][k].y = b[0].y*CP.c112[(i*3+0)*5+k] + b[1].y*CP.c112[(i*3+1)*5+k] + b[2].y*CP.c112[(i*3+2)*5+k];
-            }
-#pragma unroll
-          for (int u = 0; u < 8; ++u) {
-            float2 P[5];
-#pragma unroll
-            for (int k = 0; k < 5; ++k) {
-              P[k].x = a[u][0].x*bt[0][k].x + a[u][1].x*bt[1][k].x + a[u][2].x*bt[2][k].x;
-              P[k].y = a[u][0].y*bt[0][k].y + a[u][1].y*bt[1][k].y + a[u][2].y*bt[2][k].y;
-            }
-            float4 wl = lds4[(uc*8+u)*32 + v];
-#pragma unroll
-            for (int k = 0; k < 5; ++k) {
-              y[0][k].x += P[k].x*wl.x; y[0][k].y += P[k].y*wl.x;
-              y[1][k].x += P[k].x*wl.y; y[1][k].y += P[k].y*wl.y;
-              y[2][k].x += P[k].x*wl.z; y[2][k].y += P[k].y*wl.z;
-              y[3][k].x += P[k].x*wl.w; y[3][k].y += P[k].y*wl.w;
-            }
-          }
-        }
-      }
-    }
-
-    {
-      const float4* W4 = (const float4*)(W + 557056);
-      __syncthreads();
-      for (int t = tid; t < 256; t += 128) lds4[t] = W4[t*4 + w04];
-      __syncthreads();
+    __syncthreads();
+    for (int t = tid; t < 1024; t += 128)
+      lds4[t] = ((const float4*)W)[81920 + t*4 + w04];
+    __syncthreads();
+    for (int uc = 0; uc < 4; ++uc) {
+      float2 a[16];
+#pragma unroll
+      for (int u = 0; u < 16; ++u) LDA2(a[u], uc*16 + u);
       for (int v = 0; v < 16; ++v) {
         float2 b[5];
 #pragma unroll
         for (int j = 0; j < 5; ++j) LDB2(b[j], 160 + v*5 + j);
-        float2 bt[5][5];
-#pragma unroll
-        for (int i = 0; i < 5; ++i)
+        float2 bc[5];
+#pragma unroll
+        for (int k = 0; k < 5; ++k) {
+          float tx = 0.f, ty = 0.f;
+#pragma unroll
+          for (int j = 0; j < 5; ++j) { tx += b[j].x*CS.c022[j*5+k]; ty += b[j].y*CS.c022[j*5+k]; }
+          bc[k].x = tx; bc[k].y = ty;
+        }
+        float2 g[4];
+#pragma unroll
+        for (int w = 0; w < 4; w++) g[w] = make_float2(0.f, 0.f);
+#pragma unroll
+        for (int u = 0; u < 16; ++u) {
+          float4 wl = lds4[(uc*16+u)*16 + v];
+          g[0].x += a[u].x*wl.x; g[0].y += a[u].y*wl.x;
+          g[1].x += a[u].x*wl.y; g[1].y += a[u].y*wl.y;
+          g[2].x += a[u].x*wl.z; g[2].y += a[u].y*wl.z;
+          g[3].x += a[u].x*wl.w; g[3].y += a[u].y*wl.w;
+        }
+#pragma unroll
+        for (int w = 0; w < 4; ++w)
 #pragma unroll
           for (int k = 0; k < 5; ++k) {
-            float tx = 0.f, ty = 0.f;
-#pragma unroll
-            for (int j = 0; j < 5; ++j) { tx += b[j].x*CP.c222[(i*5+j)*5+k]; ty += b[j].y*CP.c222[(i*5+j)*5+k]; }
-            bt[i][k].x = tx; bt[i][k].y = ty;
-          }
-        for (int u = 0; u < 16; ++u) {
-          float2 aa[5];
-#pragma unroll
-          for (int i = 0; i < 5; ++i) LDA2(aa[i], 160 + u*5 + i);
+            y[w][k].x += bc[k].x*g[w].x; y[w][k].y += bc[k].y*g[w].y;
+          }
+      }
+    }
+
+    __syncthreads();
+    for (int t = tid; t < 1024; t += 128)
+      lds4[t] = ((const float4*)W)[126976 + t*4 + w04];
+    __syncthreads();
+    for (int vc = 0; vc < 4; ++vc) {
+      float2 bv[16];
+#pragma unroll
+      for (int v2 = 0; v2 < 16; ++v2) LDB2(bv[v2], vc*16 + v2);
+      for (int u = 0; u < 16; ++u) {
+        float2 aa[5];
+#pragma unroll
+        for (int i = 0; i < 5; ++i) LDA2(aa[i], 160 + u*5 + i);
+        float2 ac[5];
+#pragma unroll
+        for (int k = 0; k < 5; ++k) {
+          float tx = 0.f, ty = 0.f;
+#pragma unroll
+          for (int i = 0; i < 5; ++i) { tx += aa[i].x*CS.c202[i*5+k]; ty += aa[i].y*CS.c202[i*5+k]; }
+          ac[k].x = tx; ac[k].y = ty;
+        }
+        float2 gp[4];
+#pragma unroll
+        for (int w = 0; w < 4; w++) gp[w] = make_float2(0.f, 0.f);
+#pragma unroll
+        for (int v2 = 0; v2 < 16; ++v2) {
+          float4 wl = lds4[u*64 + vc*16 + v2];
+          gp[0].x += bv[v2].x*wl.x; gp[0].y += bv[v2].y*wl.x;
+          gp[1].x += bv[v2].x*wl.y; gp[1].y += bv[v2].y*wl.y;
+          gp[2].x += bv[v2].x*wl.z; gp[2].y += bv[v2].y*wl.z;
+          gp[3].x += bv[v2].x*wl.w; gp[3].y += bv[v2].y*wl.w;
+        }
+#pragma unroll
+        for (int w = 0; w < 4; ++w)
+#pragma unroll
+          for (int k = 0; k < 5; ++k) {
+            y[w][k].x += ac[k].x*gp[w].x; y[w][k].y += ac[k].y*gp[w].y;
+          }
+      }
+    }
+
+    __syncthreads();
+    for (int t = tid; t < 1024; t += 128)
+      lds4[t] = ((const float4*)W)[118784 + t*4 + w04];
+    __syncthreads();
+    for (int uc = 0; uc < 4; ++uc) {
+      float2 a[8][3];
+#pragma unroll
+      for (int u = 0; u < 8; ++u)
+#pragma unroll
+        for (int i = 0; i < 3; ++i) LDA2(a[u][i], 64 + (uc*8+u)*3 + i);
+#pragma unroll 2
+      for (int v = 0; v < 32; ++v) {
+        float2 b[3];
+#pragma unroll
+        for (int j = 0; j < 3; ++j) LDB2(b[j], 64 + v*3 + j);
+        float2 bt[3][5];
+#pragma unroll
+        for (int i = 0; i < 3; ++i)
+#pragma unroll
+          for (int k = 0; k < 5; ++k) {
+            bt[i][k].x = b[0].x*CP.c112[(i*3+0)*5+k] + b[1].x*CP.c112[(i*3+1)*5+k] + b[2].x*CP.c112[(i*3+2)*5+k];
+            bt[i][k].y = b[0].y*CP.c112[(i*3+0)*5+k] + b[1].y*CP.c112[(i*3+1)*5+k] + b[2].y*CP.c112[(i*3+2)*5+k];
+          }
+#pragma unroll
+        for (int u = 0; u < 8; ++u) {
           float2 P[5];
 #pragma unroll
           for (int k = 0; k < 5; ++k) {
-            float tx = 0.f, ty = 0.f;
-#pragma unroll
-            for (int i = 0; i < 5; ++i) { tx += aa[i].x*bt[i][k].x; ty += aa[i].y*bt[i][k].y; }
-            P[k].x = tx; P[k].y = ty;
-          }
-          float4 wl = lds4[u*16 + v];
+            P[k].x = a[u][0].x*bt[0][k].x + a[u][1].x*bt[1][k].x + a[u][2].x*bt[2][k].x;
+            P[k].y = a[u][0].y*bt[0][k].y + a[u][1].y*bt[1][k].y + a[u][2].y*bt[2][k].y;
+          }
+          float4 wl = lds4[(uc*8+u)*32 + v];
 #pragma unroll
           for (int k = 0; k < 5; ++k) {
             y[0][k].x += P[k].x*wl.x; y[0][k].y += P[k].y*wl.x;
@@ -681,6 +608,47 @@
             y[2][k].x += P[k].x*wl.z; y[2][k].y += P[k].y*wl.z;
             y[3][k].x += P[k].x*wl.w; y[3][k].y += P[k].y*wl.w;
           }
+        }
+      }
+    }
+
+    __syncthreads();
+    for (int t = tid; t < 256; t += 128)
+      lds4[t] = ((const float4*)W)[139264 + t*4 + w04];
+    __syncthreads();
+    for (int v = 0; v < 16; ++v) {
+      float2 b[5];
+#pragma unroll
+      for (int j = 0; j < 5; ++j) LDB2(b[j], 160 + v*5 + j);
+      float2 bt[5][5];
+#pragma unroll
+      for (int i = 0; i < 5; ++i)
+#pragma unroll
+        for (int k = 0; k < 5; ++k) {
+          float tx = 0.f, ty = 0.f;
+#pragma unroll
+          for (int j = 0; j < 5; ++j) { tx += b[j].x*CP.c222[(i*5+j)*5+k]; ty += b[j].y*CP.c222[(i*5+j)*5+k]; }
+          bt[i][k].x = tx; bt[i][k].y = ty;
+        }
+      for (int u = 0; u < 16; ++u) {
+        float2 aa[5];
+#pragma unroll
+        for (int i = 0; i < 5; ++i) LDA2(aa[i], 160 + u*5 + i);
+        float2 P[5];
+#pragma unroll
+        for (int k = 0; k < 5; ++k) {
+          float tx = 0.f, ty = 0.f;
+#pragma unroll
+          for (int i = 0; i < 5; ++i) { tx += aa[i].x*bt[i][k].x; ty += aa[i].y*bt[i][k].y; }
+          P[k].x = tx; P[k].y = ty;
+        }
+        float4 wl = lds4[u*16 + v];
+#pragma unroll
+        for (int k = 0; k < 5; ++k) {
+          y[0][k].x += P[k].x*wl.x; y[0][k].y += P[k].y*wl.x;
+          y[1][k].x += P[k].x*wl.y; y[1][k].y += P[k].y*wl.y;
+          y[2][k].x += P[k].x*wl.z; y[2][k].y += P[k].y*wl.z;
+          y[3][k].x += P[k].x*wl.w; y[3][k].y += P[k].y*wl.w;
         }
       }
     }
@@ -875,7 +843,7 @@
     k_edge<<<1280, 256, 0, stream>>>(ei, EA, CN, Z, AGG_NM);
     k_transpose<<<dim3(40, HD), 256, 0, stream>>>(AGG_NM, AGG_T);
     const float* Wu = w_tp_upd + (size_t)L*UPD_WS;
-    k_upd<<<dim3(40, 28), 128, 0, stream>>>(cur, AGG_T, Wu, cus, cud, cup, UPD_T);
+    k_upd<<<dim3(40, 52), 128, 0, stream>>>(cur, AGG_T, Wu, cus, cud, cup, UPD_T);
     k_apply<<<dim3(40, HD), 256, 0, stream>>>(cur, UPD_T, w_lin_upd + (size_t)L*LIN_WS, nxt);
     float* tmp = cur; cur = nxt; nxt = tmp;
   }
```
